# Optimization experiments

Hardware: AMD Instinct MI355X
Metric: run time of the kernel (lower is better)

## Reference

```python
import jax, jax.numpy as jnp
import numpy as np

NUM_LAYERS = 4


def setup_inputs() -> dict:
    key = jax.random.key(0)
    k1, k2, k3, k4 = jax.random.split(key, 4)
    num_users, num_items, D, E = 100000, 50000, 64, 2000000
    N = num_users + num_items
    emb_users = jax.random.normal(k1, (num_users, D), dtype=jnp.float32)
    emb_items = jax.random.normal(k2, (num_items, D), dtype=jnp.float32)
    src = jax.random.randint(k3, (E,), 0, N, dtype=jnp.int64)
    dst = jax.random.randint(k4, (E,), 0, N, dtype=jnp.int64)
    edge_index = jnp.stack([src, dst], axis=0)
    return {"emb_users": emb_users, "emb_items": emb_items, "edge_index": edge_index}


def _lightgcn(emb_users, emb_items, edge_index):
    num_users = emb_users.shape[0]
    num_items = emb_items.shape[0]
    N = num_users + num_items
    src, dst = edge_index[0], edge_index[1]

    # gcn_norm without self-loops (PyG LGConv default): deg over destination nodes
    ones = jnp.ones(src.shape[0], dtype=emb_users.dtype)
    deg = jax.ops.segment_sum(ones, dst, num_segments=N)
    deg_inv_sqrt = jnp.where(deg > 0, jax.lax.rsqrt(jnp.maximum(deg, 1.0)), 0.0)
    norm = deg_inv_sqrt[src] * deg_inv_sqrt[dst]  # [E]

    emb = jnp.concatenate([emb_users, emb_items], axis=0)  # [N, D]
    acc = emb
    for _ in range(NUM_LAYERS):
        msg = norm[:, None] * emb[src]  # [E, D]
        emb = jax.ops.segment_sum(msg, dst, num_segments=N)
        acc = acc + emb

    # original: 1/(L+1) * mean(stack, dim=1) == sum / (L+1)^2
    emb_final = acc / float((NUM_LAYERS + 1) ** 2)
    return emb_final[:num_users], emb_final[num_users:]


def reference(emb_users, emb_items, edge_index):
    return _lightgcn(emb_users, emb_items, edge_index)
```

## Files before the change

kernel.cpp:

```cpp
#include <hip/hip_runtime.h>
#include <hip/hip_bf16.h>

#define D 64
#define NUM_LAYERS 4
#define TILE 4096
#define EPT 16
#define BKMAX 320


__device__ __forceinline__ float bf_lo(unsigned u) { return __uint_as_float(u << 16); }
__device__ __forceinline__ float bf_hi(unsigned u) { return __uint_as_float(u & 0xffff0000u); }
__device__ __forceinline__ unsigned bf_pack(float x, float y) {
    __hip_bfloat16 bx = __float2bfloat16(x);
    __hip_bfloat16 by = __float2bfloat16(y);
    return (unsigned)(*reinterpret_cast<unsigned short*>(&bx))
         | ((unsigned)(*reinterpret_cast<unsigned short*>(&by)) << 16);
}


__global__ void bhist_kernel(const int* __restrict__ dst, int* __restrict__ bcnt, int E, int nbk) {
    __shared__ int h[BKMAX];
    for (int i = threadIdx.x; i < nbk; i += blockDim.x) h[i] = 0;
    __syncthreads();
    int stride = gridDim.x * blockDim.x;
    int gid = blockIdx.x * blockDim.x + threadIdx.x;
    int E4 = (((size_t)dst & 15) == 0) ? (E >> 2) : 0;
    const int4* dst4 = (const int4*)dst;
    for (int i = gid; i < E4; i += stride) {
        int4 d = dst4[i];
        atomicAdd(&h[d.x >> 9], 1);
        atomicAdd(&h[d.y >> 9], 1);
        atomicAdd(&h[d.z >> 9], 1);
        atomicAdd(&h[d.w >> 9], 1);
    }
    for (int e = (E4 << 2) + gid; e < E; e += stride)
        atomicAdd(&h[dst[e] >> 9], 1);
    __syncthreads();
    for (int i = threadIdx.x; i < nbk; i += blockDim.x)
        if (h[i] > 0) atomicAdd(&bcnt[i], h[i]);
}

__global__ __launch_bounds__(512) void bscan_kernel(const int* __restrict__ bcnt,
                                                    int* __restrict__ bstart,
                                                    int* __restrict__ gcur, int nbk, int E) {
    __shared__ int sm[512];
    int t = threadIdx.x;
    int v = (t < nbk) ? bcnt[t] : 0;
    sm[t] = v;
    __syncthreads();
    for (int ofs = 1; ofs < 512; ofs <<= 1) {
        int x = (t >= ofs) ? sm[t - ofs] : 0;
        __syncthreads();
        sm[t] += x;
        __syncthreads();
    }
    int excl = sm[t] - v;
    if (t < nbk) { bstart[t] = excl; gcur[t] = excl; }
    if (t == 0) bstart[nbk] = E;
}


__global__ __launch_bounds__(256) void placeA_kernel(const int* __restrict__ src,
                                                     const int* __restrict__ dst,
                                                     int* __restrict__ gcur,
                                                     int* __restrict__ mid,
                                                     int E, int nbk) {
    __shared__ int hist[BKMAX];
    __shared__ int gbase[BKMAX];
    int t = threadIdx.x;
    int tile0 = blockIdx.x * TILE;
    for (int i = t; i < nbk; i += 256) hist[i] = 0;
    __syncthreads();

    bool al = (((size_t)src & 15) == 0) && (((size_t)dst & 15) == 0);

    int p_[EPT];
    int b_[EPT];
    int r_[EPT];
#pragma unroll
    for (int i4 = 0; i4 < 4; ++i4) {
        int e0 = tile0 + i4 * 1024 + t * 4;
        int4 s4, d4;
        if (al && (e0 + 3 < E)) {
            s4 = *(const int4*)(src + e0);
            d4 = *(const int4*)(dst + e0);
        } else {
            s4 = make_int4(0, 0, 0, 0); d4 = make_int4(0, 0, 0, 0);
            if (e0     < E) { s4.x = src[e0];     d4.x = dst[e0]; }
            if (e0 + 1 < E) { s4.y = src[e0 + 1]; d4.y = dst[e0 + 1]; }
            if (e0 + 2 < E) { s4.z = src[e0 + 2]; d4.z = dst[e0 + 2]; }
            if (e0 + 3 < E) { s4.w = src[e0 + 3]; d4.w = dst[e0 + 3]; }
        }
        int ss[4] = { s4.x, s4.y, s4.z, s4.w };
        int dd[4] = { d4.x, d4.y, d4.z, d4.w };
#pragma unroll
        for (int k = 0; k < 4; ++k) {
            int i = i4 * 4 + k;
            int e = e0 + k;
            b_[i] = -1;
            if (e < E) {
                p_[i] = ss[k] | ((dd[k] & 511) << 18);
                b_[i] = dd[k] >> 9;
                r_[i] = atomicAdd(&hist[b_[i]], 1);
            }
        }
    }
    __syncthreads();
    for (int b = t; b < nbk; b += 256) {
        int h = hist[b];
        gbase[b] = (h > 0) ? atomicAdd(&gcur[b], h) : 0;
    }
    __syncthreads();
#pragma unroll
    for (int i = 0; i < EPT; ++i) {
        if (b_[i] >= 0) mid[gbase[b_[i]] + r_[i]] = p_[i];
    }
}

__global__ __launch_bounds__(512) void placeB1_kernel(const int* __restrict__ bstart,
                                                      const int* __restrict__ mid,
                                                      int* __restrict__ row_start,
                                                      float* __restrict__ dis,
                                                      int N, int nbk, int E) {
    __shared__ int degsm[512];
    __shared__ int sc[512];
    int b = blockIdx.x;
    int t = threadIdx.x;
    int node0 = b << 9;
    int lo = bstart[b], hi = bstart[b + 1];
    degsm[t] = 0;
    __syncthreads();
    for (int e = lo + t; e < hi; e += 512)
        atomicAdd(&degsm[(mid[e] >> 18) & 511], 1);
    __syncthreads();
    int d = degsm[t];
    sc[t] = d;
    __syncthreads();
    for (int ofs = 1; ofs < 512; ofs <<= 1) {
        int x = (t >= ofs) ? sc[t - ofs] : 0;
        __syncthreads();
        sc[t] += x;
        __syncthreads();
    }
    int excl = sc[t] - d;
    int node = node0 + t;
    if (node < N) {
        row_start[node] = lo + excl;
        dis[node] = (d > 0) ? rsqrtf((float)d) : 0.0f;
    }
    if (b == nbk - 1 && t == 0) row_start[N] = E;
}

__global__ __launch_bounds__(512) void placeB2_kernel(const int* __restrict__ bstart,
                                                      const int* __restrict__ mid,
                                                      const int* __restrict__ row_start,
                                                      const float* __restrict__ dis,
                                                      int2* __restrict__ csr, int N) {
    __shared__ int cur[512];
    __shared__ float dloc[512];
    int b = blockIdx.x;
    int t = threadIdx.x;
    int node0 = b << 9;
    int node = node0 + t;
    if (node < N) { cur[t] = row_start[node]; dloc[t] = dis[node]; }
    else          { cur[t] = 0; dloc[t] = 0.0f; }
    __syncthreads();
    int lo = bstart[b], hi = bstart[b + 1];
    for (int e = lo + t; e < hi; e += 512) {
        int m = mid[e];
        int l = (m >> 18) & 511;
        int s = m & 0x3FFFF;
        float w = dis[s] * dloc[l];
        int slot = atomicAdd(&cur[l], 1);
        csr[slot] = make_int2(s, __float_as_int(w));
    }
}


__global__ void init_kernel(const float* __restrict__ users, const float* __restrict__ items,
                            unsigned* __restrict__ A, int nu_elems, int total8) {
    int i = blockIdx.x * blockDim.x + threadIdx.x;
    if (i >= total8) return;
    long long base = (long long)i * 8;
    const float4* p;
    if (base < nu_elems) p = (const float4*)users + (base >> 2);
    else                 p = (const float4*)items + ((base - nu_elems) >> 2);
    float4 a = p[0];
    float4 b = p[1];
    uint4 r;
    r.x = bf_pack(a.x, a.y);
    r.y = bf_pack(a.z, a.w);
    r.z = bf_pack(b.x, b.y);
    r.w = bf_pack(b.z, b.w);
    ((uint4*)A)[i] = r;
}

template <int FINAL>
__global__ void gather_kernel(const int* __restrict__ row_start,
                              const int2* __restrict__ csr,
                              const uint2* __restrict__ Au,
                              uint2* __restrict__ Bu,
                              const float* __restrict__ users, const float* __restrict__ items,
                              const uint2* __restrict__ L1u, const uint2* __restrict__ L2u,
                              float* __restrict__ out,
                              int N, int nu) {
    int node = (blockIdx.x * blockDim.x + threadIdx.x) >> 6;
    if (node >= N) return;
    int lane = threadIdx.x & 63;
    int q = lane >> 4;
    int c = lane & 15;
    int beg = row_start[node];
    int end = row_start[node + 1];
    int deg = end - beg;
    float ax = 0.0f, ay = 0.0f, az = 0.0f, aw = 0.0f;

    for (int base = 0; base < deg; base += 64) {
        int chunk = min(64, deg - base);
        int   sl = 0;
        float wl = 0.0f;
        if (lane < chunk) {
            int2 e = csr[beg + base + lane];
            sl = e.x;
            wl = __int_as_float(e.y);
        }
        int k = 0;
        for (; k + 8 <= chunk; k += 8) {
            int i0 = k + q, i1 = k + 4 + q;
            int   s0 = __shfl(sl, i0), s1 = __shfl(sl, i1);
            float w0 = __shfl(wl, i0), w1 = __shfl(wl, i1);
            uint2 u0 = Au[(size_t)s0 * 16 + c];
            uint2 u1 = Au[(size_t)s1 * 16 + c];
            ax += w0 * bf_lo(u0.x); ay += w0 * bf_hi(u0.x);
            az += w0 * bf_lo(u0.y); aw += w0 * bf_hi(u0.y);
            ax += w1 * bf_lo(u1.x); ay += w1 * bf_hi(u1.x);
            az += w1 * bf_lo(u1.y); aw += w1 * bf_hi(u1.y);
        }
        for (; k < chunk; k += 4) {
            int i0 = k + q;
            int   s = __shfl(sl, i0);
            float w = __shfl(wl, i0);
            uint2 u = Au[(size_t)s * 16 + c];
            ax += w * bf_lo(u.x); ay += w * bf_hi(u.x);
            az += w * bf_lo(u.y); aw += w * bf_hi(u.y);
        }
    }

    ax += __shfl_xor(ax, 16); ay += __shfl_xor(ay, 16);
    az += __shfl_xor(az, 16); aw += __shfl_xor(aw, 16);
    ax += __shfl_xor(ax, 32); ay += __shfl_xor(ay, 32);
    az += __shfl_xor(az, 32); aw += __shfl_xor(aw, 32);

    if (q == 0) {
        size_t ro = (size_t)node * 16 + c;
        if (FINAL) {
            uint2 l1 = L1u[ro], l2 = L2u[ro], l3 = Au[ro];
            float4 e0;
            if (node < nu) e0 = ((const float4*)users)[ro];
            else           e0 = ((const float4*)items)[(size_t)(node - nu) * 16 + c];
            float rx = (e0.x + bf_lo(l1.x) + bf_lo(l2.x) + bf_lo(l3.x) + ax) * 0.04f;
            float ry = (e0.y + bf_hi(l1.x) + bf_hi(l2.x) + bf_hi(l3.x) + ay) * 0.04f;
            float rz = (e0.z + bf_lo(l1.y) + bf_lo(l2.y) + bf_lo(l3.y) + az) * 0.04f;
            float rw = (e0.w + bf_hi(l1.y) + bf_hi(l2.y) + bf_hi(l3.y) + aw) * 0.04f;
            ((float4*)out)[ro] = make_float4(rx, ry, rz, rw);
        } else {
            uint2 p;
            p.x = bf_pack(ax, ay);
            p.y = bf_pack(az, aw);
            Bu[ro] = p;
        }
    }
}


extern "C" void kernel_launch(void* const* d_in, const int* in_sizes, int n_in,
                              void* d_out, int out_size, void* d_ws, size_t ws_size,
                              hipStream_t stream) {
    const float* users = (const float*)d_in[0];
    const float* items = (const float*)d_in[1];
    const int*   eidx  = (const int*)d_in[2];

    const int nu = in_sizes[0] / D;
    const int ni = in_sizes[1] / D;
    const int N  = nu + ni;
    const int E  = in_sizes[2] / 2;
    const int Nf = N * D;
    const int nbk = (N + 511) >> 9;

    const int* src = eidx;
    const int* dst = eidx + E;

    char* ws = (char*)d_ws;
    size_t off = 0;
    auto alloc = [&](size_t bytes) {
        char* p = ws + off;
        off += (bytes + 255) & ~(size_t)255;
        return p;
    };
    float* dis       = (float*)alloc((size_t)N * 4);
    int*   row_start = (int*)alloc((size_t)(N + 1) * 4);
    int*   bcnt      = (int*)alloc(BKMAX * 4);
    int*   bstart    = (int*)alloc((BKMAX + 1) * 4);
    int*   gcur      = (int*)alloc(BKMAX * 4);
    int2*  csr       = (int2*)alloc((size_t)E * 8);
    unsigned* A0 = (unsigned*)alloc((size_t)Nf * 2);
    unsigned* L1 = (unsigned*)alloc((size_t)Nf * 2);
    unsigned* L2 = (unsigned*)alloc((size_t)Nf * 2);
    unsigned* L3 = (unsigned*)alloc((size_t)Nf * 2);
    int* mid = (int*)L3;

    const int B256 = 256;
    auto blocks = [](long long n, int b) { return (int)((n + b - 1) / b); };

    hipMemsetAsync(bcnt, 0, BKMAX * 4, stream);
    bhist_kernel<<<1024, B256, 0, stream>>>(dst, bcnt, E, nbk);
    bscan_kernel<<<1, 512, 0, stream>>>(bcnt, bstart, gcur, nbk, E);

    placeA_kernel<<<blocks(E, TILE), B256, 0, stream>>>(src, dst, gcur, mid, E, nbk);
    placeB1_kernel<<<nbk, 512, 0, stream>>>(bstart, mid, row_start, dis, N, nbk, E);
    placeB2_kernel<<<nbk, 512, 0, stream>>>(bstart, mid, row_start, dis, csr, N);

    init_kernel<<<blocks(Nf / 8, B256), B256, 0, stream>>>(users, items, A0, nu * D, Nf / 8);

    const int ggrid = blocks(N, B256 / 64);
    gather_kernel<0><<<ggrid, B256, 0, stream>>>(row_start, csr, (const uint2*)A0, (uint2*)L1,
                                                 nullptr, nullptr, nullptr, nullptr, nullptr, N, nu);
    gather_kernel<0><<<ggrid, B256, 0, stream>>>(row_start, csr, (const uint2*)L1, (uint2*)L2,
                                                 nullptr, nullptr, nullptr, nullptr, nullptr, N, nu);
    gather_kernel<0><<<ggrid, B256, 0, stream>>>(row_start, csr, (const uint2*)L2, (uint2*)L3,
                                                 nullptr, nullptr, nullptr, nullptr, nullptr, N, nu);
    gather_kernel<1><<<ggrid, B256, 0, stream>>>(row_start, csr, (const uint2*)L3, nullptr,
                                                 users, items, (const uint2*)L1, (const uint2*)L2,
                                                 (float*)d_out, N, nu);
}
```

Measured before the change: 396.4 us.

## Stage bucketed edges in shared memory for coalesced scatter in placeA

The bucketing kernel now does a block-local prefix scan over bucket histograms and sorts each tile's edges by bucket into shared memory before writing to the global intermediate array. Consecutive threads then write contiguous runs within each bucket, replacing the scattered per-thread writes. The block size goes to 512 threads with 8 edges per thread. In exchange it adds a 512-wide shared-memory scan with many barriers, and more shared memory per block.

```diff
diff --git a/kernel.cpp b/kernel.cpp
--- a/kernel.cpp
+++ b/kernel.cpp
@@ -4,7 +4,6 @@
 #define D 64
 #define NUM_LAYERS 4
 #define TILE 4096
-#define EPT 16
 #define BKMAX 320
 
 
@@ -60,26 +59,31 @@
 }
 
 
-__global__ __launch_bounds__(256) void placeA_kernel(const int* __restrict__ src,
+__global__ __launch_bounds__(512) void placeA_kernel(const int* __restrict__ src,
                                                      const int* __restrict__ dst,
                                                      int* __restrict__ gcur,
                                                      int* __restrict__ mid,
                                                      int E, int nbk) {
     __shared__ int hist[BKMAX];
+    __shared__ int toff[BKMAX];
     __shared__ int gbase[BKMAX];
+    __shared__ int sc[512];
+    __shared__ int els[TILE];
+    __shared__ unsigned short bkt[TILE];
     int t = threadIdx.x;
     int tile0 = blockIdx.x * TILE;
-    for (int i = t; i < nbk; i += 256) hist[i] = 0;
+    int tcnt = min(TILE, E - tile0);
+    for (int i = t; i < nbk; i += 512) hist[i] = 0;
     __syncthreads();
 
     bool al = (((size_t)src & 15) == 0) && (((size_t)dst & 15) == 0);
 
-    int p_[EPT];
-    int b_[EPT];
-    int r_[EPT];
+    int p_[8];
+    int b_[8];
+    int r_[8];
 #pragma unroll
-    for (int i4 = 0; i4 < 4; ++i4) {
-        int e0 = tile0 + i4 * 1024 + t * 4;
+    for (int i4 = 0; i4 < 2; ++i4) {
+        int e0 = tile0 + i4 * 2048 + t * 4;
         int4 s4, d4;
         if (al && (e0 + 3 < E)) {
             s4 = *(const int4*)(src + e0);
@@ -106,14 +110,33 @@
         }
     }
     __syncthreads();
-    for (int b = t; b < nbk; b += 256) {
+    int v = (t < nbk) ? hist[t] : 0;
+    sc[t] = v;
+    __syncthreads();
+    for (int ofs = 1; ofs < 512; ofs <<= 1) {
+        int x = (t >= ofs) ? sc[t - ofs] : 0;
+        __syncthreads();
+        sc[t] += x;
+        __syncthreads();
+    }
+    if (t < nbk) toff[t] = sc[t] - v;
+    __syncthreads();
+#pragma unroll
+    for (int i = 0; i < 8; ++i) {
+        if (b_[i] >= 0) {
+            int pos = toff[b_[i]] + r_[i];
+            els[pos] = p_[i];
+            bkt[pos] = (unsigned short)b_[i];
+        }
+    }
+    for (int b = t; b < nbk; b += 512) {
         int h = hist[b];
         gbase[b] = (h > 0) ? atomicAdd(&gcur[b], h) : 0;
     }
     __syncthreads();
-#pragma unroll
-    for (int i = 0; i < EPT; ++i) {
-        if (b_[i] >= 0) mid[gbase[b_[i]] + r_[i]] = p_[i];
+    for (int i = t; i < tcnt; i += 512) {
+        int b = bkt[i];
+        mid[gbase[b] + (i - toff[b])] = els[i];
     }
 }
 
@@ -315,7 +338,7 @@
     bhist_kernel<<<1024, B256, 0, stream>>>(dst, bcnt, E, nbk);
     bscan_kernel<<<1, 512, 0, stream>>>(bcnt, bstart, gcur, nbk, E);
 
-    placeA_kernel<<<blocks(E, TILE), B256, 0, stream>>>(src, dst, gcur, mid, E, nbk);
+    placeA_kernel<<<blocks(E, TILE), 512, 0, stream>>>(src, dst, gcur, mid, E, nbk);
     placeB1_kernel<<<nbk, 512, 0, stream>>>(bstart, mid, row_start, dis, N, nbk, E);
     placeB2_kernel<<<nbk, 512, 0, stream>>>(bstart, mid, row_start, dis, csr, N);
 
```

New measurement: 390.7 us (median of 2 runs). Within noise of the previous version (-1.4%).
